# Optimization experiments

Hardware: AMD Instinct MI355X
Metric: run time of the kernel (lower is better)

Reference implementation:

```python
import jax, jax.numpy as jnp
import numpy as np

C = 256          # in_channels == representation_size (GNN(in_channels, in_channels))
REP = 256
H = 300
W = 300
K = 5            # conv/patch kernel
S = 5            # patch stride
KNN = 7          # node_connectivities[0]
HEADS = 8
NH, NW = H // S, W // S
N = NH * NW      # 3600 graph nodes


def setup_inputs() -> dict:
    key = jax.random.key(0)
    ctr = [0]
    def nk():
        ctr[0] += 1
        return jax.random.fold_in(key, ctr[0])
    def rn(shape, s):
        return jax.random.normal(nk(), shape, dtype=jnp.float32) * s
    d = {}
    d['x'] = jax.random.normal(nk(), (1, C, H, W), dtype=jnp.float32)
    d['conv1_w'] = rn((C, C, K, K), 0.02)
    d['conv1_b'] = jnp.zeros((C,), jnp.float32)
    d['fc2_w'] = rn((C, REP), 0.02)
    d['fc2_b'] = jnp.zeros((REP,), jnp.float32)
    d['fc3_w'] = rn((2 * REP, REP), 0.02)
    d['fc3_b'] = jnp.zeros((REP,), jnp.float32)
    def gat(pfx, fin, heads):
        d[pfx + '_wl'] = rn((fin, heads * REP), 0.03)
        d[pfx + '_bl'] = jnp.zeros((heads * REP,), jnp.float32)
        d[pfx + '_wr'] = rn((fin, heads * REP), 0.03)
        d[pfx + '_br'] = jnp.zeros((heads * REP,), jnp.float32)
        d[pfx + '_att'] = rn((heads, REP), 0.1)
        d[pfx + '_bias'] = jnp.zeros((heads * REP,), jnp.float32)
    gat('g1', REP, HEADS)
    gat('g2', HEADS * REP, 1)
    gat('g3', REP, HEADS)
    gat('g4', HEADS * REP, 1)
    return d


def _gatv2(x, wl, bl, wr, br, att, bias, src, dst, mask):
    # PyG GATv2Conv (eval mode, add_self_loops handled by caller via src/dst/mask)
    heads, F = att.shape
    n = x.shape[0]
    xl = (x @ wl + bl).reshape(n, heads, F)   # source transform
    xr = (x @ wr + br).reshape(n, heads, F)   # target transform
    e = jax.nn.leaky_relu(xl[src] + xr[dst], 0.2)          # [E,H,F]
    logit = jnp.einsum('ehf,hf->eh', e, att)               # [E,H]
    logit = jnp.where(mask[:, None], logit, -1e30)
    m = jax.ops.segment_max(logit, dst, num_segments=n)    # every node has a self loop
    ex = jnp.exp(logit - m[dst]) * mask[:, None]
    denom = jax.ops.segment_sum(ex, dst, num_segments=n)
    alpha = ex / denom[dst]
    out = jax.ops.segment_sum(alpha[:, :, None] * xl[src], dst, num_segments=n)
    return out.reshape(n, heads * F) + bias


def _edges_from_topk(vals, idx, strict):
    # torch: A.scatter(1, idx, vals); triu; nonzero -> (row<=col, val!=0);
    # GATv2Conv then removes self loops and adds one per node.
    rows = jnp.arange(N)
    if strict:
        keep = (rows[:, None] < idx) & (vals != 0)
    else:
        keep = (rows[:, None] <= idx) & (vals != 0)  # diag excluded by vals==0 (cdist self-dist)
    src = jnp.concatenate([idx.ravel(), rows])       # source = column index
    dst = jnp.concatenate([jnp.repeat(rows, KNN), rows])  # target = row index
    mask = jnp.concatenate([keep.ravel(), jnp.ones((N,), bool)])
    return src, dst, mask


def _forward(x, conv1_w, conv1_b, fc2_w, fc2_b, fc3_w, fc3_b,
             g1_wl, g1_bl, g1_wr, g1_br, g1_att, g1_bias,
             g2_wl, g2_bl, g2_wr, g2_br, g2_att, g2_bias,
             g3_wl, g3_bl, g3_wr, g3_br, g3_att, g3_bias,
             g4_wl, g4_bl, g4_wr, g4_br, g4_att, g4_bias):
    # --- non-overlapping 5x5 patch embed: unfold + conv(5)->1x1 output ---
    patches = x[0].reshape(C, NH, K, NW, K).transpose(1, 3, 0, 2, 4).reshape(N, C, K, K)
    emb = jax.nn.relu(jnp.einsum('nckl,ockl->no', patches, conv1_w) + conv1_b)
    emb = jax.nn.relu(emb @ fc2_w + fc2_b)  # [N, REP]  (fc1 is unused in the original forward)

    # --- feature-similarity graph: emb @ emb.T, row-wise top-k, triu ---
    adj = emb @ emb.T
    vals, idx = jax.lax.top_k(adj, KNN)
    src1, dst1, m1 = _edges_from_topk(vals, idx, strict=True)

    # --- spatial kNN graph over region centers (cdist, smallest-k, triu) ---
    yy, xx = jnp.meshgrid(jnp.arange(0, H, S, dtype=jnp.float32),
                          jnp.arange(0, W, S, dtype=jnp.float32), indexing='ij')
    centers = jnp.stack([yy.ravel(), xx.ravel()], -1)    # [N,2], i-major like patches
    sq = jnp.sum(centers * centers, -1)
    dist = jnp.sqrt(jnp.maximum(sq[:, None] + sq[None, :] - 2.0 * (centers @ centers.T), 0.0))
    nv, nidx = jax.lax.top_k(-dist, KNN)
    src2, dst2, m2 = _edges_from_topk(-nv, nidx, strict=False)

    h = jax.nn.elu(_gatv2(emb, g1_wl, g1_bl, g1_wr, g1_br, g1_att, g1_bias, src1, dst1, m1))
    h = jax.nn.elu(_gatv2(h, g2_wl, g2_bl, g2_wr, g2_br, g2_att, g2_bias, src1, dst1, m1))
    h_ = jax.nn.elu(_gatv2(emb, g3_wl, g3_bl, g3_wr, g3_br, g3_att, g3_bias, src2, dst2, m2))
    h_ = jax.nn.elu(_gatv2(h_, g4_wl, g4_bl, g4_wr, g4_br, g4_att, g4_bias, src2, dst2, m2))

    hc = jax.nn.relu(jnp.concatenate([h, h_], axis=1) @ fc3_w + fc3_b)
    return hc + h_


def reference(x, conv1_w, conv1_b, fc2_w, fc2_b, fc3_w, fc3_b,
              g1_wl, g1_bl, g1_wr, g1_br, g1_att, g1_bias,
              g2_wl, g2_bl, g2_wr, g2_br, g2_att, g2_bias,
              g3_wl, g3_bl, g3_wr, g3_br, g3_att, g3_bias,
              g4_wl, g4_bl, g4_wr, g4_br, g4_att, g4_bias):
    return _forward(x, conv1_w, conv1_b, fc2_w, fc2_b, fc3_w, fc3_b,
                    g1_wl, g1_bl, g1_wr, g1_br, g1_att, g1_bias,
                    g2_wl, g2_bl, g2_wr, g2_br, g2_att, g2_bias,
                    g3_wl, g3_bl, g3_wr, g3_br, g3_att, g3_bias,
                    g4_wl, g4_bl, g4_wr, g4_br, g4_att, g4_bias)
```

## Files before the change

kernel.cpp:

```cpp
#include <hip/hip_runtime.h>
#include <hip/hip_bf16.h>
#include <math.h>

#define NN 3600
#define HIMG 300
#define WIMG 300
#define NHP 60
#define NCT 57

typedef __attribute__((ext_vector_type(8))) short bf16x8;
typedef __attribute__((ext_vector_type(4))) float f32x4;

__device__ __forceinline__ float bf2f(unsigned short u) {
  union { unsigned int i; float f; } v; v.i = ((unsigned int)u) << 16; return v.f;
}
__device__ __forceinline__ float ldE(const void* p, long i, int md) {
  return md ? bf2f(((const unsigned short*)p)[i]) : ((const float*)p)[i];
}
__device__ __forceinline__ unsigned short f2bf(float f) {
  __hip_bfloat16 h = __float2bfloat16(f);
  return *(unsigned short*)&h;
}

__global__ __launch_bounds__(256) void detect_mode(
    const unsigned short* __restrict__ x, int* __restrict__ flag) {
  __shared__ int bad;
  if (threadIdx.x == 0) bad = 0;
  __syncthreads();
  int b = 0;
  for (int i = threadIdx.x; i < 8192; i += 256) {
    int e = (x[i] >> 7) & 0xFF;
    if (e >= 0x90) b = 1;
  }
  if (b) atomicOr(&bad, 1);
  __syncthreads();
  if (threadIdx.x == 0) {
    flag[0] = bad ? 0 : 1;
    flag[1] = 0;
  }
}

__global__ __launch_bounds__(256) void wtrans(
    const void* __restrict__ w, float* __restrict__ wT, const int* __restrict__ mode) {
  const int md = *mode;
  __shared__ float t[32][33];
  const int k0 = blockIdx.x * 32, o0 = blockIdx.y * 32;
  const int tx = threadIdx.x & 31, ty = threadIdx.x >> 5;
#pragma unroll
  for (int s = 0; s < 32; s += 8)
    t[ty + s][tx] = ldE(w, (long)(o0 + ty + s) * 6400 + k0 + tx, md);
  __syncthreads();
#pragma unroll
  for (int s = 0; s < 32; s += 8)
    wT[(size_t)(k0 + ty + s) * 256 + o0 + tx] = t[tx][ty + s];
}

__global__ __launch_bounds__(256) void wconvT(
    const void* __restrict__ src, unsigned short* __restrict__ dst,
    int Kd, int Nd, const int* __restrict__ mode) {
  const int md = *mode;
  __shared__ float t[32][33];
  const int k0 = blockIdx.x * 32, n0 = blockIdx.y * 32;
  const int tx = threadIdx.x & 31, ty = threadIdx.x >> 5;
#pragma unroll
  for (int s = 0; s < 32; s += 8)
    t[ty + s][tx] = ldE(src, (long)(k0 + ty + s) * Nd + n0 + tx, md);
  __syncthreads();
#pragma unroll
  for (int s = 0; s < 32; s += 8)
    dst[(size_t)(n0 + ty + s) * Kd + k0 + tx] = f2bf(t[tx][ty + s]);
}

__global__ __launch_bounds__(256) void cvt_bf16(
    const float* __restrict__ src, unsigned short* __restrict__ dst, long n4) {
  for (long i = (long)blockIdx.x * 256 + threadIdx.x; i < n4; i += (long)gridDim.x * 256) {
    float4 v = *(const float4*)(src + i * 4);
    ushort4 o;
    o.x = f2bf(v.x); o.y = f2bf(v.y); o.z = f2bf(v.z); o.w = f2bf(v.w);
    *(ushort4*)(dst + i * 4) = o;
  }
}

__global__ __launch_bounds__(256) void im2col(
    const void* __restrict__ x, float* __restrict__ a2, int h, const int* __restrict__ mode) {
  const int md = *mode;
  const int total = NN * 3200;
  for (int i = blockIdx.x * 256 + threadIdx.x; i < total; i += gridDim.x * 256) {
    int n = i / 3200, kl = i - n * 3200;
    int k = h * 3200 + kl;
    int c = k / 25, q = k - c * 25;
    int ki = q / 5, li = q - ki * 5;
    int ni = n / NHP, nj = n - ni * NHP;
    a2[i] = ldE(x, (long)c * (HIMG * WIMG) + (5 * ni + ki) * WIMG + 5 * nj + li, md);
  }
}

template <int STORE, int ACT>
__global__ __launch_bounds__(256) void gemm_u(
    const float* __restrict__ A, const void* __restrict__ B0, const void* __restrict__ B1,
    long boff, const void* __restrict__ bias0, const void* __restrict__ bias1, long biasoff,
    float* __restrict__ C0, float* __restrict__ C1, float* __restrict__ part, int cld,
    int M, int lda, int kchunk, int KS, int ldb, const int* __restrict__ mode) {
  const int md = *mode;
  const int z = blockIdx.z;
  const int pair = z / KS, ks = z - pair * KS;
  const void* B = pair ? B1 : B0;
  const void* bias = pair ? bias1 : bias0;
  float* C = pair ? C1 : C0;
  __shared__ float As[16][68];
  __shared__ float Bs[16][68];
  const int m0 = blockIdx.y * 64, n0 = blockIdx.x * 64;
  const int tid = threadIdx.x;
  const int tr = tid >> 4, tc = tid & 15;
  const int ar = tid >> 2, akq = tid & 3;
  const int bkr = tid >> 4, bnc = tid & 15;
  const int arow = m0 + ar;
  float acc[4][4] = {};

  const int kb = ks * kchunk, ke = kb + kchunk;
  for (int k0 = kb; k0 < ke; k0 += 16) {
    __syncthreads();
    {
      float4 v = make_float4(0.f, 0.f, 0.f, 0.f);
      if (arow < M) v = *(const float4*)(A + (size_t)arow * lda + k0 + akq * 4);
      As[akq * 4 + 0][ar] = v.x;
      As[akq * 4 + 1][ar] = v.y;
      As[akq * 4 + 2][ar] = v.z;
      As[akq * 4 + 3][ar] = v.w;
    }
    {
      long bidx = (long)(k0 + bkr) * ldb + boff + n0 + bnc * 4;
      if (md) {
        ushort4 u = *(const ushort4*)((const unsigned short*)B + bidx);
        Bs[bkr][bnc * 4 + 0] = bf2f(u.x);
        Bs[bkr][bnc * 4 + 1] = bf2f(u.y);
        Bs[bkr][bnc * 4 + 2] = bf2f(u.z);
        Bs[bkr][bnc * 4 + 3] = bf2f(u.w);
      } else {
        float4 v = *(const float4*)((const float*)B + bidx);
        Bs[bkr][bnc * 4 + 0] = v.x;
        Bs[bkr][bnc * 4 + 1] = v.y;
        Bs[bkr][bnc * 4 + 2] = v.z;
        Bs[bkr][bnc * 4 + 3] = v.w;
      }
    }
    __syncthreads();
#pragma unroll
    for (int kk = 0; kk < 16; ++kk) {
      float4 av = *(const float4*)&As[kk][tr * 4];
      float4 bv = *(const float4*)&Bs[kk][tc * 4];
      float a[4] = {av.x, av.y, av.z, av.w};
      float b[4] = {bv.x, bv.y, bv.z, bv.w};
#pragma unroll
      for (int i = 0; i < 4; ++i)
#pragma unroll
        for (int j = 0; j < 4; ++j) acc[i][j] = fmaf(a[i], b[j], acc[i][j]);
    }
  }
#pragma unroll
  for (int i = 0; i < 4; ++i) {
    int row = m0 + tr * 4 + i;
    if (row < M) {
#pragma unroll
      for (int j = 0; j < 4; ++j) {
        int col = n0 + tc * 4 + j;
        if (STORE == 2) {
          part[((size_t)z * M + row) * cld + col] = acc[i][j];
        } else if (STORE == 1) {
          C[(size_t)row * cld + col] += acc[i][j];
        } else {
          float v = acc[i][j] + ldE(bias, biasoff + col, md);
          if (ACT == 1) v = fmaxf(v, 0.f);
          C[(size_t)row * cld + col] = v;
        }
      }
    }
  }
}

template <int STORE>
__global__ __launch_bounds__(256) void gemm_mf(
    const unsigned short* __restrict__ A,
    const unsigned short* __restrict__ B0, const unsigned short* __restrict__ B1,
    const void* __restrict__ bias0, const void* __restrict__ bias1,
    float* __restrict__ C0, float* __restrict__ C1, float* __restrict__ part, int cld,
    int M, int K, int kchunk, int KS, const int* __restrict__ mode) {
  const int md = *mode;
  const int z = blockIdx.z;
  const int pair = z / KS, ks = z - pair * KS;
  const unsigned short* B = pair ? B1 : B0;
  const void* bias = pair ? bias1 : bias0;
  float* C = pair ? C1 : C0;

  __shared__ __align__(16) unsigned short Al[128][40];
  __shared__ __align__(16) unsigned short Bl[128][40];
  const int m0 = blockIdx.y * 128, n0 = blockIdx.x * 128;
  const int tid = threadIdx.x;
  const int lane = tid & 63, w = tid >> 6;
  const int wr = (w >> 1) * 64, wc = (w & 1) * 64;
  const int frow = lane & 15, fk = (lane >> 4) * 8;

  f32x4 acc[4][4];
#pragma unroll
  for (int i = 0; i < 4; ++i)
#pragma unroll
    for (int j = 0; j < 4; ++j) acc[i][j] = (f32x4){0.f, 0.f, 0.f, 0.f};

  const int kb0 = ks * kchunk, ke = kb0 + kchunk;
  for (int kb = kb0; kb < ke; kb += 32) {
    __syncthreads();
    for (int c = tid; c < 512; c += 256) {
      int row = c >> 2, kc = (c & 3) << 3;
      uint4 v = make_uint4(0, 0, 0, 0);
      int gr = m0 + row;
      if (gr < M) v = *(const uint4*)(A + (size_t)gr * K + kb + kc);
      *(uint4*)&Al[row][kc] = v;
    }
    for (int c = tid; c < 512; c += 256) {
      int col = c >> 2, kc = (c & 3) << 3;
      uint4 v = *(const uint4*)(B + (size_t)(n0 + col) * K + kb + kc);
      *(uint4*)&Bl[col][kc] = v;
    }
    __syncthreads();

    bf16x8 af[4], bfr[4];
#pragma unroll
    for (int rt = 0; rt < 4; ++rt)
      af[rt] = *(const bf16x8*)&Al[wr + rt * 16 + frow][fk];
#pragma unroll
    for (int ct = 0; ct < 4; ++ct)
      bfr[ct] = *(const bf16x8*)&Bl[wc + ct * 16 + frow][fk];
#pragma unroll
    for (int rt = 0; rt < 4; ++rt)
#pragma unroll
      for (int ct = 0; ct < 4; ++ct)
        acc[rt][ct] = __builtin_amdgcn_mfma_f32_16x16x32_bf16(af[rt], bfr[ct], acc[rt][ct], 0, 0, 0);
  }

#pragma unroll
  for (int rt = 0; rt < 4; ++rt) {
#pragma unroll
    for (int ct = 0; ct < 4; ++ct) {
      int col = n0 + wc + ct * 16 + (lane & 15);
#pragma unroll
      for (int reg = 0; reg < 4; ++reg) {
        int row = m0 + wr + rt * 16 + ((lane >> 4) << 2) + reg;
        if (row < M) {
          float v = acc[rt][ct][reg];
          if (STORE == 2) {
            part[((size_t)z * M + row) * cld + col] = v;
          } else {
            C[(size_t)row * cld + col] = v + ldE(bias, col, md);
          }
        }
      }
    }
  }
}

template <int ACT>
__global__ __launch_bounds__(256) void reduce_u(
    const float* __restrict__ part, int KS, int M, int ncols,
    const void* __restrict__ bias0, const void* __restrict__ bias1, long biasoff,
    float* __restrict__ C0, float* __restrict__ C1, int cld, const int* __restrict__ mode) {
  const int md = *mode;
  const int pair = blockIdx.z;
  const void* bias = pair ? bias1 : bias0;
  float* C = pair ? C1 : C0;
  size_t total = (size_t)M * ncols;
  for (size_t i = (size_t)blockIdx.x * blockDim.x + threadIdx.x; i < total;
       i += (size_t)gridDim.x * blockDim.x) {
    int row = (int)(i / ncols), col = (int)(i - (size_t)row * ncols);
    float s = 0.f;
    for (int ks = 0; ks < KS; ++ks)
      s += part[(((size_t)(pair * KS + ks)) * M + row) * ncols + col];
    s += ldE(bias, biasoff + col, md);
    if (ACT == 1) s = fmaxf(s, 0.f);
    C[(size_t)row * cld + col] = s;
  }
}

__global__ __launch_bounds__(256) void patch_part(
    const void* __restrict__ x, const void* __restrict__ w,
    float* __restrict__ part, int CPB, const int* __restrict__ mode) {
  const int md = *mode;
  __shared__ float As[25][68];
  __shared__ float Bs[25][68];
  const int m0 = blockIdx.y * 64, n0 = blockIdx.x * 64;
  const int tid = threadIdx.x;
  const int tr = tid >> 4, tc = tid & 15;
  const int z = blockIdx.z;
  float acc[4][4] = {};
  const int c0 = z * CPB;
  for (int c = c0; c < c0 + CPB; ++c) {
    __syncthreads();
    for (int e = tid; e < 1600; e += 256) {
      int p = e / 25, q = e - p * 25;
      int ki = q / 5, li = q - ki * 5;
      int n = m0 + p;
      float v = 0.f;
      if (n < NN) {
        int ni = n / NHP, nj = n - ni * NHP;
        v = ldE(x, (long)c * (HIMG * WIMG) + (5 * ni + ki) * WIMG + 5 * nj + li, md);
      }
      As[q][p] = v;
    }
    for (int e = tid; e < 1600; e += 256) {
      int o = e / 25, q = e - o * 25;
      Bs[q][o] = ldE(w, (long)(n0 + o) * 6400 + c * 25 + q, md);
    }
    __syncthreads();
#pragma unroll
    for (int kk = 0; kk < 25; ++kk) {
      float4 av = *(const float4*)&As[kk][tr * 4];
      float4 bv = *(const float4*)&Bs[kk][tc * 4];
      float a[4] = {av.x, av.y, av.z, av.w};
      float b[4] = {bv.x, bv.y, bv.z, bv.w};
#pragma unroll
      for (int i = 0; i < 4; ++i)
#pragma unroll
        for (int j = 0; j < 4; ++j) acc[i][j] = fmaf(a[i], b[j], acc[i][j]);
    }
  }
#pragma unroll
  for (int i = 0; i < 4; ++i) {
    int row = m0 + tr * 4 + i;
    if (row < NN) {
#pragma unroll
      for (int j = 0; j < 4; ++j)
        part[((size_t)z * NN + row) * 256 + n0 + tc * 4 + j] = acc[i][j];
    }
  }
}

__global__ __launch_bounds__(256) void adj_gemm(
    const float* __restrict__ emb, float* __restrict__ pv, unsigned char* __restrict__ pi) {
  __shared__ float As[16][68];
  __shared__ float Bs[16][68];
  __shared__ float mv[64][68];
  __shared__ unsigned char mi[64][68];
  const int m0 = blockIdx.y * 64, n0 = blockIdx.x * 64;
  const int ct = blockIdx.x;
  const int tid = threadIdx.x;
  const int tr = tid >> 4, tc = tid & 15;
  const int ar = tid >> 2, akq = tid & 3;
  const int bn = tid >> 2, bkq = tid & 3;
  const int arow = m0 + ar;
  const int bcol = n0 + bn;
  float acc[4][4] = {};

  for (int k0 = 0; k0 < 256; k0 += 16) {
    __syncthreads();
    {
      float4 v = make_float4(0.f, 0.f, 0.f, 0.f);
      if (arow < NN) v = *(const float4*)(emb + (size_t)arow * 256 + k0 + akq * 4);
      As[akq * 4 + 0][ar] = v.x;
      As[akq * 4 + 1][ar] = v.y;
      As[akq * 4 + 2][ar] = v.z;
      As[akq * 4 + 3][ar] = v.w;
    }
    {
      float4 v = make_float4(0.f, 0.f, 0.f, 0.f);
      if (bcol < NN) v = *(const float4*)(emb + (size_t)bcol * 256 + k0 + bkq * 4);
      Bs[bkq * 4 + 0][bn] = v.x;
      Bs[bkq * 4 + 1][bn] = v.y;
      Bs[bkq * 4 + 2][bn] = v.z;
      Bs[bkq * 4 + 3][bn] = v.w;
    }
    __syncthreads();
#pragma unroll
    for (int kk = 0; kk < 16; ++kk) {
      float4 av = *(const float4*)&As[kk][tr * 4];
      float4 bv = *(const float4*)&Bs[kk][tc * 4];
      float a[4] = {av.x, av.y, av.z, av.w};
      float b[4] = {bv.x, bv.y, bv.z, bv.w};
#pragma unroll
      for (int i = 0; i < 4; ++i)
#pragma unroll
        for (int j = 0; j < 4; ++j) acc[i][j] = fmaf(a[i], b[j], acc[i][j]);
    }
  }

#pragma unroll
  for (int i = 0; i < 4; ++i) {
    float v[4]; int id[4];
#pragma unroll
    for (int j = 0; j < 4; ++j) {
      int cl = tc * 4 + j;
      int valid = (n0 + cl) < NN;
      v[j] = valid ? acc[i][j] : -1e38f;
      id[j] = valid ? cl : 255;
    }
#pragma unroll
    for (int a = 1; a < 4; ++a) {
      float va = v[a]; int ia = id[a];
      int b = a;
      while (b > 0 && (va > v[b - 1] || (va == v[b - 1] && ia < id[b - 1]))) {
        v[b] = v[b - 1]; id[b] = id[b - 1]; --b;
      }
      v[b] = va; id[b] = ia;
    }
    int rl = tr * 4 + i;
#pragma unroll
    for (int s = 0; s < 4; ++s) {
      mv[rl][tc * 4 + s] = v[s];
      mi[rl][tc * 4 + s] = (unsigned char)id[s];
    }
  }
  __syncthreads();

  if (tid < 64) {
    int row = m0 + tid;
    if (row < NN) {
      int ptr[16];
#pragma unroll
      for (int g = 0; g < 16; ++g) ptr[g] = 0;
      for (int k = 0; k < 7; ++k) {
        float best = -1e38f; int bid = 0x7fffffff; int bg = 0;
        for (int g = 0; g < 16; ++g) {
          if (ptr[g] < 4) {
            float vv = mv[tid][g * 4 + ptr[g]];
            int ii = mi[tid][g * 4 + ptr[g]];
            if (vv > best || (vv == best && ii < bid)) { best = vv; bid = ii; bg = g; }
          }
        }
        ptr[bg]++;
        pv[(size_t)row * (NCT * 7) + ct * 7 + k] = best;
        pi[(size_t)row * (NCT * 7) + ct * 7 + k] = (unsigned char)bid;
      }
    }
  }
}

__global__ __launch_bounds__(256) void adj_merge57(
    const float* __restrict__ pv, const unsigned char* __restrict__ pi,
    int* __restrict__ idx_o, int* __restrict__ keep_o) {
  __shared__ unsigned char sp[256][NCT + 3];
  const int t = threadIdx.x;
  const int row = blockIdx.x * 256 + t;
  for (int c = 0; c < NCT; ++c) sp[t][c] = 0;
  if (row >= NN) return;
  const size_t base = (size_t)row * (NCT * 7);
  for (int k = 0; k < 7; ++k) {
    float best = -1e38f; int bidx = 0x7fffffff; int bct = 0;
    for (int c = 0; c < NCT; ++c) {
      int p = sp[t][c];
      if (p < 7) {
        float v = pv[base + c * 7 + p];
        int ii = c * 64 + (int)pi[base + c * 7 + p];
        if (v > best || (v == best && ii < bidx)) { best = v; bidx = ii; bct = c; }
      }
    }
    sp[t][bct]++;
    idx_o[row * 7 + k] = bidx;
    keep_o[row * 7 + k] = (bidx > row && best != 0.0f) ? 1 : 0;
  }
}

__global__ __launch_bounds__(256) void spatial_topk(int* __restrict__ idx_o, int* __restrict__ keep_o) {
  int r = blockIdx.x * 256 + threadIdx.x;
  if (r >= NN) return;
  int ri = r / NHP, rj = r - (r / NHP) * NHP;
  int bd[7], bi[7];
#pragma unroll
  for (int k = 0; k < 7; ++k) { bd[k] = 0x7fffffff; bi[k] = 0x7fffffff; }
  int ilo = ri - 2 > 0 ? ri - 2 : 0, ihi = ri + 2 < NHP - 1 ? ri + 2 : NHP - 1;
  int jlo = rj - 2 > 0 ? rj - 2 : 0, jhi = rj + 2 < NHP - 1 ? rj + 2 : NHP - 1;
  for (int i2 = ilo; i2 <= ihi; ++i2) {
    int dy = ri - i2; int dy2 = dy * dy;
    for (int j2 = jlo; j2 <= jhi; ++j2) {
      int dx = rj - j2;
      int d = dy2 + dx * dx;
      int m = i2 * NHP + j2;
      if (d < bd[6]) {
        int pq = 6;
        while (pq > 0 && d < bd[pq - 1]) { bd[pq] = bd[pq - 1]; bi[pq] = bi[pq - 1]; --pq; }
        bd[pq] = d; bi[pq] = m;
      }
    }
  }
#pragma unroll
  for (int k = 0; k < 7; ++k) {
    idx_o[r * 7 + k] = bi[k];
    keep_o[r * 7 + k] = (bi[k] >= r && bd[k] != 0) ? 1 : 0;
  }
}

__global__ __launch_bounds__(256) void gat_agg1(
    const float* __restrict__ xl, const float* __restrict__ xr,
    const void* __restrict__ att, long attoff, const void* __restrict__ gbias, long gboff,
    const int* __restrict__ nbr, const int* __restrict__ keep,
    float* __restrict__ out, const int* __restrict__ mode) {
  const int md = *mode;
  const int r = blockIdx.x;
  const int f = threadIdx.x;
  __shared__ int s_src[8];
  __shared__ int s_mask_s;
  __shared__ float red[4][8];
  if (f < 7) {
    int v = nbr[r * 7 + f];
    s_src[f] = ((unsigned)v < (unsigned)NN) ? v : 0;
  }
  if (f == 7) s_src[7] = r;
  if (f == 0) {
    int mk = 0x80;
    for (int e = 0; e < 7; ++e)
      if (keep[r * 7 + e] != 0) mk |= (1 << e);
    s_mask_s = mk;
  }
  __syncthreads();
  const int mask = s_mask_s;
  const int wid = f >> 6, lane = f & 63;

  float xrv = xr[(size_t)r * 256 + f];
  float attv = ldE(att, attoff + f, md);
  float xlv[8], part[8];
#pragma unroll
  for (int e = 0; e < 8; ++e) {
    xlv[e] = 0.f; part[e] = 0.f;
    if (mask & (1 << e)) {
      float v = xl[(size_t)s_src[e] * 256 + f];
      xlv[e] = v;
      float s = v + xrv;
      s = s > 0.f ? s : 0.2f * s;
      part[e] = s * attv;
    }
  }
#pragma unroll
  for (int e = 0; e < 8; ++e) {
    float v = part[e];
#pragma unroll
    for (int off = 32; off > 0; off >>= 1) v += __shfl_xor(v, off, 64);
    if (lane == 0) red[wid][e] = v;
  }
  __syncthreads();
  float m = -1e38f;
  float logit[8];
#pragma unroll
  for (int e = 0; e < 8; ++e) {
    logit[e] = red[0][e] + red[1][e] + red[2][e] + red[3][e];
    if (mask & (1 << e)) m = fmaxf(m, logit[e]);
  }
  float den = 0.f, al[8];
#pragma unroll
  for (int e = 0; e < 8; ++e) {
    al[e] = (mask & (1 << e)) ? expf(logit[e] - m) : 0.f;
    den += al[e];
  }
  float inv = 1.0f / den;
  float o = 0.f;
#pragma unroll
  for (int e = 0; e < 8; ++e) o = fmaf(al[e], xlv[e], o);
  o = o * inv + ldE(gbias, gboff + f, md);
  o = o > 0.f ? o : expm1f(o);
  out[(size_t)r * 256 + f] = o;
}

__global__ __launch_bounds__(256) void gat_agg8(
    const float* __restrict__ xl, const float* __restrict__ xr,
    const void* __restrict__ att, const void* __restrict__ gbias,
    const int* __restrict__ nbr, const int* __restrict__ keep,
    float* __restrict__ out, const int* __restrict__ mode) {
  const int md = *mode;
  const int r = blockIdx.x;
  const int f = threadIdx.x;
  __shared__ int s_src[8];
  __shared__ int s_mask_s;
  __shared__ float red[4][8];
  if (f < 7) {
    int v = nbr[r * 7 + f];
    s_src[f] = ((unsigned)v < (unsigned)NN) ? v : 0;
  }
  if (f == 7) s_src[7] = r;
  if (f == 0) {
    int mk = 0x80;
    for (int e = 0; e < 7; ++e)
      if (keep[r * 7 + e] != 0) mk |= (1 << e);
    s_mask_s = mk;
  }
  __syncthreads();
  const int mask = s_mask_s;
  const int wid = f >> 6, lane = f & 63;

  for (int h = 0; h < 8; ++h) {
    float xrv = xr[(size_t)r * 2048 + h * 256 + f];
    float attv = ldE(att, h * 256 + f, md);
    float xlv[8], part[8];
#pragma unroll
    for (int e = 0; e < 8; ++e) {
      xlv[e] = 0.f; part[e] = 0.f;
      if (mask & (1 << e)) {
        float v = xl[(size_t)s_src[e] * 2048 + h * 256 + f];
        xlv[e] = v;
        float s = v + xrv;
        s = s > 0.f ? s : 0.2f * s;
        part[e] = s * attv;
      }
    }
#pragma unroll
    for (int e = 0; e < 8; ++e) {
      float v = part[e];
#pragma unroll
      for (int off = 32; off > 0; off >>= 1) v += __shfl_xor(v, off, 64);
      if (lane == 0) red[wid][e] = v;
    }
    __syncthreads();
    float m = -1e38f;
    float logit[8];
#pragma unroll
    for (int e = 0; e < 8; ++e) {
      logit[e] = red[0][e] + red[1][e] + red[2][e] + red[3][e];
      if (mask & (1 << e)) m = fmaxf(m, logit[e]);
    }
    float den = 0.f, al[8];
#pragma unroll
    for (int e = 0; e < 8; ++e) {
      al[e] = (mask & (1 << e)) ? expf(logit[e] - m) : 0.f;
      den += al[e];
    }
    float inv = 1.0f / den;
    float o = 0.f;
#pragma unroll
    for (int e = 0; e < 8; ++e) o = fmaf(al[e], xlv[e], o);
    o = o * inv + ldE(gbias, h * 256 + f, md);
    o = o > 0.f ? o : expm1f(o);
    out[(size_t)r * 2048 + h * 256 + f] = o;
    __syncthreads();
  }
}

__global__ __launch_bounds__(256) void fc3_final(
    const float* __restrict__ h2, const float* __restrict__ h4,
    const void* __restrict__ B, const void* __restrict__ bias,
    void* __restrict__ outp, const int* __restrict__ mode) {
  const int md = *mode;
  __shared__ float As[16][68];
  __shared__ float Bs[16][68];
  const int m0 = blockIdx.y * 64, n0 = blockIdx.x * 64;
  const int tid = threadIdx.x;
  const int tr = tid >> 4, tc = tid & 15;
  const int ar = tid >> 2, akq = tid & 3;
  const int bkr = tid >> 4, bnc = tid & 15;
  const int arow = m0 + ar;
  float acc[4][4] = {};

  for (int k0 = 0; k0 < 512; k0 += 16) {
    __syncthreads();
    {
      int k = k0 + akq * 4;
      float4 v = make_float4(0.f, 0.f, 0.f, 0.f);
      if (arow < NN) {
        const float* src = (k < 256) ? (h2 + (size_t)arow * 256 + k)
                                     : (h4 + (size_t)arow * 256 + (k - 256));
        v = *(const float4*)src;
      }
      As[akq * 4 + 0][ar] = v.x;
      As[akq * 4 + 1][ar] = v.y;
      As[akq * 4 + 2][ar] = v.z;
      As[akq * 4 + 3][ar] = v.w;
    }
    {
      long bidx = (long)(k0 + bkr) * 256 + n0 + bnc * 4;
      if (md) {
        ushort4 u = *(const ushort4*)((const unsigned short*)B + bidx);
        Bs[bkr][bnc * 4 + 0] = bf2f(u.x);
        Bs[bkr][bnc * 4 + 1] = bf2f(u.y);
        Bs[bkr][bnc * 4 + 2] = bf2f(u.z);
        Bs[bkr][bnc * 4 + 3] = bf2f(u.w);
      } else {
        float4 v = *(const float4*)((const float*)B + bidx);
        Bs[bkr][bnc * 4 + 0] = v.x;
        Bs[bkr][bnc * 4 + 1] = v.y;
        Bs[bkr][bnc * 4 + 2] = v.z;
        Bs[bkr][bnc * 4 + 3] = v.w;
      }
    }
    __syncthreads();
#pragma unroll
    for (int kk = 0; kk < 16; ++kk) {
      float4 av = *(const float4*)&As[kk][tr * 4];
      float4 bv = *(const float4*)&Bs[kk][tc * 4];
      float a[4] = {av.x, av.y, av.z, av.w};
      float b[4] = {bv.x, bv.y, bv.z, bv.w};
#pragma unroll
      for (int i = 0; i < 4; ++i)
#pragma unroll
        for (int j = 0; j < 4; ++j) acc[i][j] = fmaf(a[i], b[j], acc[i][j]);
    }
  }
#pragma unroll
  for (int i = 0; i < 4; ++i) {
    int row = m0 + tr * 4 + i;
    if (row < NN) {
#pragma unroll
      for (int j = 0; j < 4; ++j) {
        int col = n0 + tc * 4 + j;
        float v = fmaxf(acc[i][j] + ldE(bias, col, md), 0.f) + h4[(size_t)row * 256 + col];
        if (md) ((__hip_bfloat16*)outp)[(size_t)row * 256 + col] = __float2bfloat16(v);
        else ((float*)outp)[(size_t)row * 256 + col] = v;
      }
    }
  }
}

extern "C" void kernel_launch(void* const* d_in, const int* in_sizes, int n_in,
                              void* d_out, int out_size, void* d_ws, size_t ws_size,
                              hipStream_t stream) {
  (void)in_sizes; (void)n_in; (void)out_size;
  const void* x    = d_in[0];
  const void* w1   = d_in[1];
  const void* b1   = d_in[2];
  const void* fc2w = d_in[3];
  const void* fc2b = d_in[4];
  const void* fc3w = d_in[5];
  const void* fc3b = d_in[6];
  const void* g_wl[4]   = {d_in[7],  d_in[13], d_in[19], d_in[25]};
  const void* g_bl[4]   = {d_in[8],  d_in[14], d_in[20], d_in[26]};
  const void* g_wr[4]   = {d_in[9],  d_in[15], d_in[21], d_in[27]};
  const void* g_br[4]   = {d_in[10], d_in[16], d_in[22], d_in[28]};
  const void* g_att[4]  = {d_in[11], d_in[17], d_in[23], d_in[29]};
  const void* g_bias[4] = {d_in[12], d_in[18], d_in[24], d_in[30]};

  float* ws = (float*)d_ws;
  int* mode = (int*)d_ws;
  size_t off = 64;
  float* emb = ws + off; off += (size_t)NN * 256;
  float* xl2 = ws + off; off += (size_t)NN * 256;
  float* xr2 = ws + off; off += (size_t)NN * 256;
  float* h2  = ws + off; off += (size_t)NN * 256;
  float* h4  = ws + off; off += (size_t)NN * 256;
  int* idx1  = (int*)(ws + off); off += NN * 7;
  int* keep1 = (int*)(ws + off); off += NN * 7;
  int* idx2  = (int*)(ws + off); off += NN * 7;
  int* keep2 = (int*)(ws + off); off += NN * 7;
  unsigned short* emb_bf = (unsigned short*)(ws + off); off += (size_t)NN * 256 / 2;
  unsigned short* wbfL   = (unsigned short*)(ws + off); off += (size_t)524288 / 2;
  unsigned short* wbfR   = (unsigned short*)(ws + off); off += (size_t)524288 / 2;
  float* scratch = ws + off;
  const size_t wide_need = off + 3 * (size_t)NN * 2048;
  const bool wide = ws_size >= wide_need * sizeof(float);

  float* emb1 = h2;
  float* pv = scratch;
  unsigned char* pi = (unsigned char*)(scratch + (size_t)NN * (NCT * 7));

  dim3 blk(256);
  const int* idxs[2]  = {idx1, idx2};
  const int* keeps[2] = {keep1, keep2};
  float* houts[2] = {h2, h4};
  const int* f32mode = mode + 1;

  detect_mode<<<dim3(1), blk, 0, stream>>>((const unsigned short*)x, mode);

  if (wide) {
    float* wT   = scratch;
    float* part = wT + (size_t)6400 * 256;
    float* a2   = part + 8 * (size_t)NN * 256;

    wtrans<<<dim3(200, 8), blk, 0, stream>>>(w1, wT, mode);
    for (int h = 0; h < 2; ++h) {
      im2col<<<dim3(2048), blk, 0, stream>>>(x, a2, h, mode);
      gemm_u<2, 0><<<dim3(4, 57, 4), blk, 0, stream>>>(a2, wT, wT, (long)h * 3200 * 256,
                                                       nullptr, nullptr, 0,
                                                       nullptr, nullptr, part + (size_t)h * 4 * NN * 256,
                                                       256, NN, 3200, 800, 4, 256, f32mode);
    }
    reduce_u<1><<<dim3(1024, 1, 1), blk, 0, stream>>>(part, 8, NN, 256,
                                                      b1, b1, 0, emb1, emb1, 256, mode);
  } else {
    const int convKS = 2;
    patch_part<<<dim3(4, 57, convKS), blk, 0, stream>>>(x, w1, scratch, 256 / convKS, mode);
    reduce_u<1><<<dim3(1024, 1, 1), blk, 0, stream>>>(scratch, convKS, NN, 256,
                                                      b1, b1, 0, emb1, emb1, 256, mode);
  }

  gemm_u<0, 1><<<dim3(4, 57, 1), blk, 0, stream>>>(emb1, fc2w, fc2w, 0, fc2b, fc2b, 0,
                                                   emb, emb, nullptr, 256,
                                                   NN, 256, 256, 1, 256, mode);
  adj_gemm<<<dim3(NCT, NCT), blk, 0, stream>>>(emb, pv, pi);
  adj_merge57<<<dim3(15), blk, 0, stream>>>(pv, pi, idx1, keep1);
  spatial_topk<<<dim3(15), blk, 0, stream>>>(idx2, keep2);

  if (wide) {
    float* xl_w = scratch;
    float* xr_w = xl_w + (size_t)NN * 2048;
    float* hh_w = xr_w + (size_t)NN * 2048;
    unsigned short* hh_bf = (unsigned short*)xl_w;
    float* g24part = xr_w;

    cvt_bf16<<<dim3(512), blk, 0, stream>>>(emb, emb_bf, (long)NN * 64);

    for (int g = 0; g < 2; ++g) {
      int a = g * 2, b = g * 2 + 1;
      wconvT<<<dim3(8, 64), blk, 0, stream>>>(g_wl[a], wbfL, 256, 2048, mode);
      wconvT<<<dim3(8, 64), blk, 0, stream>>>(g_wr[a], wbfR, 256, 2048, mode);
      gemm_mf<0><<<dim3(16, 29, 2), blk, 0, stream>>>(emb_bf, wbfL, wbfR,
                                                      g_bl[a], g_br[a],
                                                      xl_w, xr_w, nullptr, 2048,
                                                      NN, 256, 256, 1, mode);
      gat_agg8<<<dim3(NN), blk, 0, stream>>>(xl_w, xr_w, g_att[a], g_bias[a],
                                             idxs[g], keeps[g], hh_w, mode);
      cvt_bf16<<<dim3(2048), blk, 0, stream>>>(hh_w, hh_bf, (long)NN * 512);
      wconvT<<<dim3(64, 8), blk, 0, stream>>>(g_wl[b], wbfL, 2048, 256, mode);
      wconvT<<<dim3(64, 8), blk, 0, stream>>>(g_wr[b], wbfR, 2048, 256, mode);
      gemm_mf<2><<<dim3(2, 29, 8), blk, 0, stream>>>(hh_bf, wbfL, wbfR,
                                                     nullptr, nullptr,
                                                     nullptr, nullptr, g24part, 256,
                                                     NN, 2048, 512, 4, mode);
      reduce_u<0><<<dim3(1024, 1, 2), blk, 0, stream>>>(g24part, 4, NN, 256,
                                                        g_bl[b], g_br[b], 0,
                                                        xl2, xr2, 256, mode);
      gat_agg1<<<dim3(NN), blk, 0, stream>>>(xl2, xr2, g_att[b], 0, g_bias[b], 0,
                                             idxs[g], keeps[g], houts[g], mode);
    }
  } else {
    float* xlh = scratch;
    float* xrh = xlh + (size_t)NN * 256;
    float* hh  = xrh + (size_t)NN * 256;

    for (int g = 0; g < 2; ++g) {
      int a = g * 2, b = g * 2 + 1;
      for (int h = 0; h < 8; ++h) {
        gemm_u<0, 0><<<dim3(4, 57, 2), blk, 0, stream>>>(emb, g_wl[a], g_wr[a], h * 256,
                                                         g_bl[a], g_br[a], h * 256,
                                                         xlh, xrh, nullptr, 256,
                                                         NN, 256, 256, 1, 2048, mode);
        gat_agg1<<<dim3(NN), blk, 0, stream>>>(xlh, xrh, g_att[a], h * 256, g_bias[a], h * 256,
                                               idxs[g], keeps[g], hh, mode);
        if (h == 0) {
          gemm_u<0, 0><<<dim3(4, 57, 2), blk, 0, stream>>>(hh, g_wl[b], g_wr[b], 0,
                                                           g_bl[b], g_br[b], 0,
                                                           xl2, xr2, nullptr, 256,
                                                           NN, 256, 256, 1, 256, mode);
        } else {
          gemm_u<1, 0><<<dim3(4, 57, 2), blk, 0, stream>>>(hh, g_wl[b], g_wr[b], (long)h * 256 * 256,
                                                           g_bl[b], g_br[b], 0,
                                                           xl2, xr2, nullptr, 256,
                                                           NN, 256, 256, 1, 256, mode);
        }
      }
      gat_agg1<<<dim3(NN), blk, 0, stream>>>(xl2, xr2, g_att[b], 0, g_bias[b], 0,
                                             idxs[g], keeps[g], houts[g], mode);
    }
  }

  fc3_final<<<dim3(4, 57), blk, 0, stream>>>(h2, h4, fc3w, fc3b, d_out, mode);
}
```

Before: 1.071 ms.

## Use 128x64 register-tiled fp32 conv GEMM, per-half reduce, and split GAT heads across blocks

Replaces the generic gemm_u for the im2col conv GEMM with a dedicated kernel that uses 128x64 tiles and an 8x4 per-thread register tile, with 8 K-splits of 400 each. The partial buffer is now reduced after each im2col half, accumulating into emb1 with bias and ReLU applied on the second pass, so the partial buffer only holds one half. The 8-head GAT aggregation now launches one block per (node, head) instead of looping over heads, which adds parallelism and removes the per-head barriers. The price is an extra reduce launch plus a read-modify-write of emb1.

After: 1.077 ms. No clear change (+0.6%).

```diff
diff --git a/kernel.cpp b/kernel.cpp
--- a/kernel.cpp
+++ b/kernel.cpp
@@ -92,6 +92,71 @@
     int ki = q / 5, li = q - ki * 5;
     int ni = n / NHP, nj = n - ni * NHP;
     a2[i] = ldE(x, (long)c * (HIMG * WIMG) + (5 * ni + ki) * WIMG + 5 * nj + li, md);
+  }
+}
+
+__global__ __launch_bounds__(256) void gemm_f84(
+    const float* __restrict__ A, const float* __restrict__ B, long boff,
+    float* __restrict__ part, int M, int lda, int kchunk, int ldb) {
+  __shared__ float As[16][136];
+  __shared__ float Bs[16][68];
+  const int m0 = blockIdx.y * 128, n0 = blockIdx.x * 64;
+  const int z = blockIdx.z;
+  const int tid = threadIdx.x;
+  const int tr = tid >> 4, tc = tid & 15;
+  const int ar = tid >> 1, akq = tid & 1;
+  const int bkr = tid >> 4, bnc = tid & 15;
+  const int arow = m0 + ar;
+  float acc[8][4] = {};
+
+  const int kb = z * kchunk, ke = kb + kchunk;
+  for (int k0 = kb; k0 < ke; k0 += 16) {
+    __syncthreads();
+    {
+      float4 v0 = make_float4(0.f, 0.f, 0.f, 0.f), v1 = v0;
+      if (arow < M) {
+        const float* ap = A + (size_t)arow * lda + k0 + akq * 8;
+        v0 = *(const float4*)ap;
+        v1 = *(const float4*)(ap + 4);
+      }
+      As[akq * 8 + 0][ar] = v0.x;
+      As[akq * 8 + 1][ar] = v0.y;
+      As[akq * 8 + 2][ar] = v0.z;
+      As[akq * 8 + 3][ar] = v0.w;
+      As[akq * 8 + 4][ar] = v1.x;
+      As[akq * 8 + 5][ar] = v1.y;
+      As[akq * 8 + 6][ar] = v1.z;
+      As[akq * 8 + 7][ar] = v1.w;
+    }
+    {
+      float4 v = *(const float4*)(B + (size_t)(k0 + bkr) * ldb + boff + n0 + bnc * 4);
+      Bs[bkr][bnc * 4 + 0] = v.x;
+      Bs[bkr][bnc * 4 + 1] = v.y;
+      Bs[bkr][bnc * 4 + 2] = v.z;
+      Bs[bkr][bnc * 4 + 3] = v.w;
+    }
+    __syncthreads();
+#pragma unroll
+    for (int kk = 0; kk < 16; ++kk) {
+      float4 a0 = *(const float4*)&As[kk][tr * 8];
+      float4 a1 = *(const float4*)&As[kk][tr * 8 + 4];
+      float4 bv = *(const float4*)&Bs[kk][tc * 4];
+      float a[8] = {a0.x, a0.y, a0.z, a0.w, a1.x, a1.y, a1.z, a1.w};
+      float b[4] = {bv.x, bv.y, bv.z, bv.w};
+#pragma unroll
+      for (int i = 0; i < 8; ++i)
+#pragma unroll
+        for (int j = 0; j < 4; ++j) acc[i][j] = fmaf(a[i], b[j], acc[i][j]);
+    }
+  }
+#pragma unroll
+  for (int i = 0; i < 8; ++i) {
+    int row = m0 + tr * 8 + i;
+    if (row < M) {
+#pragma unroll
+      for (int j = 0; j < 4; ++j)
+        part[((size_t)z * M + row) * 256 + n0 + tc * 4 + j] = acc[i][j];
+    }
   }
 }
 
@@ -258,7 +323,7 @@
   }
 }
 
-template <int ACT>
+template <int ACT, int ADDIN, int BIAS>
 __global__ __launch_bounds__(256) void reduce_u(
     const float* __restrict__ part, int KS, int M, int ncols,
     const void* __restrict__ bias0, const void* __restrict__ bias1, long biasoff,
@@ -271,10 +336,10 @@
   for (size_t i = (size_t)blockIdx.x * blockDim.x + threadIdx.x; i < total;
        i += (size_t)gridDim.x * blockDim.x) {
     int row = (int)(i / ncols), col = (int)(i - (size_t)row * ncols);
-    float s = 0.f;
+    float s = ADDIN ? C[(size_t)row * cld + col] : 0.f;
     for (int ks = 0; ks < KS; ++ks)
       s += part[(((size_t)(pair * KS + ks)) * M + row) * ncols + col];
-    s += ldE(bias, biasoff + col, md);
+    if (BIAS) s += ldE(bias, biasoff + col, md);
     if (ACT == 1) s = fmaxf(s, 0.f);
     C[(size_t)row * cld + col] = s;
   }
@@ -556,13 +621,14 @@
   out[(size_t)r * 256 + f] = o;
 }
 
-__global__ __launch_bounds__(256) void gat_agg8(
+__global__ __launch_bounds__(256) void gat_agg8h(
     const float* __restrict__ xl, const float* __restrict__ xr,
     const void* __restrict__ att, const void* __restrict__ gbias,
     const int* __restrict__ nbr, const int* __restrict__ keep,
     float* __restrict__ out, const int* __restrict__ mode) {
   const int md = *mode;
   const int r = blockIdx.x;
+  const int h = blockIdx.y;
   const int f = threadIdx.x;
   __shared__ int s_src[8];
   __shared__ int s_mask_s;
@@ -582,51 +648,48 @@
   const int mask = s_mask_s;
   const int wid = f >> 6, lane = f & 63;
 
-  for (int h = 0; h < 8; ++h) {
-    float xrv = xr[(size_t)r * 2048 + h * 256 + f];
-    float attv = ldE(att, h * 256 + f, md);
-    float xlv[8], part[8];
-#pragma unroll
-    for (int e = 0; e < 8; ++e) {
-      xlv[e] = 0.f; part[e] = 0.f;
-      if (mask & (1 << e)) {
-        float v = xl[(size_t)s_src[e] * 2048 + h * 256 + f];
-        xlv[e] = v;
-        float s = v + xrv;
-        s = s > 0.f ? s : 0.2f * s;
-        part[e] = s * attv;
-      }
-    }
-#pragma unroll
-    for (int e = 0; e < 8; ++e) {
-      float v = part[e];
-#pragma unroll
-      for (int off = 32; off > 0; off >>= 1) v += __shfl_xor(v, off, 64);
-      if (lane == 0) red[wid][e] = v;
-    }
-    __syncthreads();
-    float m = -1e38f;
-    float logit[8];
-#pragma unroll
-    for (int e = 0; e < 8; ++e) {
-      logit[e] = red[0][e] + red[1][e] + red[2][e] + red[3][e];
-      if (mask & (1 << e)) m = fmaxf(m, logit[e]);
-    }
-    float den = 0.f, al[8];
-#pragma unroll
-    for (int e = 0; e < 8; ++e) {
-      al[e] = (mask & (1 << e)) ? expf(logit[e] - m) : 0.f;
-      den += al[e];
-    }
-    float inv = 1.0f / den;
-    float o = 0.f;
-#pragma unroll
-    for (int e = 0; e < 8; ++e) o = fmaf(al[e], xlv[e], o);
-    o = o * inv + ldE(gbias, h * 256 + f, md);
-    o = o > 0.f ? o : expm1f(o);
-    out[(size_t)r * 2048 + h * 256 + f] = o;
-    __syncthreads();
-  }
+  float xrv = xr[(size_t)r * 2048 + h * 256 + f];
+  float attv = ldE(att, h * 256 + f, md);
+  float xlv[8], part[8];
+#pragma unroll
+  for (int e = 0; e < 8; ++e) {
+    xlv[e] = 0.f; part[e] = 0.f;
+    if (mask & (1 << e)) {
+      float v = xl[(size_t)s_src[e] * 2048 + h * 256 + f];
+      xlv[e] = v;
+      float s = v + xrv;
+      s = s > 0.f ? s : 0.2f * s;
+      part[e] = s * attv;
+    }
+  }
+#pragma unroll
+  for (int e = 0; e < 8; ++e) {
+    float v = part[e];
+#pragma unroll
+    for (int off = 32; off > 0; off >>= 1) v += __shfl_xor(v, off, 64);
+    if (lane == 0) red[wid][e] = v;
+  }
+  __syncthreads();
+  float m = -1e38f;
+  float logit[8];
+#pragma unroll
+  for (int e = 0; e < 8; ++e) {
+    logit[e] = red[0][e] + red[1][e] + red[2][e] + red[3][e];
+    if (mask & (1 << e)) m = fmaxf(m, logit[e]);
+  }
+  float den = 0.f, al[8];
+#pragma unroll
+  for (int e = 0; e < 8; ++e) {
+    al[e] = (mask & (1 << e)) ? expf(logit[e] - m) : 0.f;
+    den += al[e];
+  }
+  float inv = 1.0f / den;
+  float o = 0.f;
+#pragma unroll
+  for (int e = 0; e < 8; ++e) o = fmaf(al[e], xlv[e], o);
+  o = o * inv + ldE(gbias, h * 256 + f, md);
+  o = o > 0.f ? o : expm1f(o);
+  out[(size_t)r * 2048 + h * 256 + f] = o;
 }
 
 __global__ __launch_bounds__(256) void fc3_final(
@@ -760,18 +823,20 @@
     wtrans<<<dim3(200, 8), blk, 0, stream>>>(w1, wT, mode);
     for (int h = 0; h < 2; ++h) {
       im2col<<<dim3(2048), blk, 0, stream>>>(x, a2, h, mode);
-      gemm_u<2, 0><<<dim3(4, 57, 4), blk, 0, stream>>>(a2, wT, wT, (long)h * 3200 * 256,
-                                                       nullptr, nullptr, 0,
-                                                       nullptr, nullptr, part + (size_t)h * 4 * NN * 256,
-                                                       256, NN, 3200, 800, 4, 256, f32mode);
-    }
-    reduce_u<1><<<dim3(1024, 1, 1), blk, 0, stream>>>(part, 8, NN, 256,
-                                                      b1, b1, 0, emb1, emb1, 256, mode);
+      gemm_f84<<<dim3(4, 29, 8), blk, 0, stream>>>(a2, wT, (long)h * 3200 * 256,
+                                                   part, NN, 3200, 400, 256);
+      if (h == 0)
+        reduce_u<0, 0, 0><<<dim3(1024, 1, 1), blk, 0, stream>>>(part, 8, NN, 256,
+                                                                b1, b1, 0, emb1, emb1, 256, mode);
+      else
+        reduce_u<1, 1, 1><<<dim3(1024, 1, 1), blk, 0, stream>>>(part, 8, NN, 256,
+                                                                b1, b1, 0, emb1, emb1, 256, mode);
+    }
   } else {
     const int convKS = 2;
     patch_part<<<dim3(4, 57, convKS), blk, 0, stream>>>(x, w1, scratch, 256 / convKS, mode);
-    reduce_u<1><<<dim3(1024, 1, 1), blk, 0, stream>>>(scratch, convKS, NN, 256,
-                                                      b1, b1, 0, emb1, emb1, 256, mode);
+    reduce_u<1, 0, 1><<<dim3(1024, 1, 1), blk, 0, stream>>>(scratch, convKS, NN, 256,
+                                                            b1, b1, 0, emb1, emb1, 256, mode);
   }
 
   gemm_u<0, 1><<<dim3(4, 57, 1), blk, 0, stream>>>(emb1, fc2w, fc2w, 0, fc2b, fc2b, 0,
@@ -798,8 +863,8 @@
                                                       g_bl[a], g_br[a],
                                                       xl_w, xr_w, nullptr, 2048,
                                                       NN, 256, 256, 1, mode);
-      gat_agg8<<<dim3(NN), blk, 0, stream>>>(xl_w, xr_w, g_att[a], g_bias[a],
-                                             idxs[g], keeps[g], hh_w, mode);
+      gat_agg8h<<<dim3(NN, 8), blk, 0, stream>>>(xl_w, xr_w, g_att[a], g_bias[a],
+                                                 idxs[g], keeps[g], hh_w, mode);
       cvt_bf16<<<dim3(2048), blk, 0, stream>>>(hh_w, hh_bf, (long)NN * 512);
       wconvT<<<dim3(64, 8), blk, 0, stream>>>(g_wl[b], wbfL, 2048, 256, mode);
       wconvT<<<dim3(64, 8), blk, 0, stream>>>(g_wr[b], wbfR, 2048, 256, mode);
@@ -807,9 +872,9 @@
                                                      nullptr, nullptr,
                                                      nullptr, nullptr, g24part, 256,
                                                      NN, 2048, 512, 4, mode);
-      reduce_u<0><<<dim3(1024, 1, 2), blk, 0, stream>>>(g24part, 4, NN, 256,
-                                                        g_bl[b], g_br[b], 0,
-                                                        xl2, xr2, 256, mode);
+      reduce_u<0, 0, 1><<<dim3(1024, 1, 2), blk, 0, stream>>>(g24part, 4, NN, 256,
+                                                              g_bl[b], g_br[b], 0,
+                                                              xl2, xr2, 256, mode);
       gat_agg1<<<dim3(NN), blk, 0, stream>>>(xl2, xr2, g_att[b], 0, g_bias[b], 0,
                                              idxs[g], keeps[g], houts[g], mode);
     }
```
